# Optimization experiments

Measured on AMD Instinct MI355X. Metric: run time of the kernel, lower is better.

## Reference

```python
import jax, jax.numpy as jnp
import numpy as np

D, F, E, K = 1024, 2752, 8, 2  # hidden, intermediate, num_experts, top-k


def setup_inputs() -> dict:
    key = jax.random.key(0)
    k0, k1, k2, k3, k4 = jax.random.split(key, 5)
    s = 0.02  # init scale to keep activations in a sane range
    x = jax.random.normal(k0, (2, 512, D), jnp.float32)
    Ws = jax.random.normal(k1, (D, E), jnp.float32) * s
    bs = jnp.zeros((E,), jnp.float32)
    Wg = jax.random.normal(k2, (E, D, F), jnp.float32) * s
    Wu = jax.random.normal(k3, (E, D, F), jnp.float32) * s
    Wd = jax.random.normal(k4, (E, F, D), jnp.float32) * s
    return {"x": x, "Ws": Ws, "bs": bs, "Wg": Wg, "Wu": Wu, "Wd": Wd}


def reference(x, Ws, bs, Wg, Wu, Wd):
    b, n, d = x.shape
    xt = x.reshape(-1, d)                      # [T, D], T = b*n
    # gating: top-k over expert logits, softmax over the selected k
    logits = xt @ Ws + bs                      # [T, E]
    topk_w, topk_idx = jax.lax.top_k(logits, K)
    topk_w = jax.nn.softmax(topk_w, axis=-1)   # [T, K]
    # combine weights: zero for unselected experts
    combine = jnp.sum(jax.nn.one_hot(topk_idx, E, dtype=xt.dtype) * topk_w[..., None], axis=1)  # [T, E]
    # per-expert SwiGLU MLP (Llama): down(silu(gate(x)) * up(x))
    g = jnp.einsum('td,edf->tef', xt, Wg)
    u = jnp.einsum('td,edf->tef', xt, Wu)
    h = jax.nn.silu(g) * u                     # [T, E, F]
    y = jnp.einsum('tef,efd->ted', h, Wd)      # [T, E, D]
    out = jnp.einsum('ted,te->td', y, combine) # weighted combine over selected experts
    return out.reshape(b, n, d)
```

## Files before the change

kernel.cpp:

```cpp
#include <hip/hip_runtime.h>

#define DH 1024
#define FH 2752
#define NE 8
#define NT 1024
#define BM 256
#define BKF 64
#define BNF 32

typedef unsigned short u16;
typedef __bf16 bf16x8 __attribute__((ext_vector_type(8)));
typedef u16 u16x8 __attribute__((ext_vector_type(8)));
typedef float f32x4 __attribute__((ext_vector_type(4)));

__device__ __forceinline__ u16 f2bf(float f) {
  unsigned int u = __float_as_uint(f);
  unsigned int r = (u + 0x7fffu + ((u >> 16) & 1u)) >> 16;
  return (u16)r;
}
__device__ __forceinline__ float bf2f(u16 b) {
  return __uint_as_float(((unsigned int)b) << 16);
}
__device__ __forceinline__ bf16x8 as_bf(int4 v) {
  union { int4 i; bf16x8 b; } u; u.i = v; return u.b;
}
__device__ __forceinline__ bf16x8 as_bfu(u16x8 v) {
  union { u16x8 u; bf16x8 b; } x; x.u = v; return x.b;
}

__global__ void gate_kernel(const float* __restrict__ x,
                            const float* __restrict__ Ws,
                            const float* __restrict__ bs,
                            u16* __restrict__ xb,
                            int* __restrict__ tki,
                            float* __restrict__ tkw) {
  int gtid = blockIdx.x * blockDim.x + threadIdx.x;
  int t = gtid >> 6;
  int lane = gtid & 63;
  if (t >= NT) return;
  const float* xr = x + (size_t)t * DH;
  float acc[NE];
#pragma unroll
  for (int e = 0; e < NE; ++e) acc[e] = 0.f;
  for (int d = lane; d < DH; d += 64) {
    float xv = xr[d];
    xb[(size_t)t * DH + d] = f2bf(xv);
    const float4* wr = (const float4*)(Ws + (size_t)d * NE);
    float4 w0 = wr[0], w1 = wr[1];
    acc[0] += xv * w0.x; acc[1] += xv * w0.y;
    acc[2] += xv * w0.z; acc[3] += xv * w0.w;
    acc[4] += xv * w1.x; acc[5] += xv * w1.y;
    acc[6] += xv * w1.z; acc[7] += xv * w1.w;
  }
#pragma unroll
  for (int e = 0; e < NE; ++e) {
#pragma unroll
    for (int off = 32; off > 0; off >>= 1)
      acc[e] += __shfl_xor(acc[e], off);
  }
  if (lane == 0) {
    float l[NE];
#pragma unroll
    for (int e = 0; e < NE; ++e) l[e] = acc[e] + bs[e];
    int i0 = 0;
#pragma unroll
    for (int e = 1; e < NE; ++e) if (l[e] > l[i0]) i0 = e;
    int i1 = (i0 == 0) ? 1 : 0;
#pragma unroll
    for (int e = 0; e < NE; ++e) if (e != i0 && l[e] > l[i1]) i1 = e;
    float e1 = __expf(l[i1] - l[i0]);
    float denom = 1.f + e1;
    tki[t*2]   = i0; tki[t*2+1] = i1;
    tkw[t*2]   = 1.f / denom;
    tkw[t*2+1] = e1 / denom;
  }
}

__global__ void group_kernel(const int* __restrict__ tki,
                             int* __restrict__ offs,
                             int* __restrict__ rtok,
                             int* __restrict__ posf) {
  __shared__ int cnt[NE];
  __shared__ int run[NE];
  int tid = threadIdx.x;
  if (tid < NE) cnt[tid] = 0;
  __syncthreads();
  for (int t = tid; t < NT; t += blockDim.x) {
    atomicAdd(&cnt[tki[t*2]], 1);
    atomicAdd(&cnt[tki[t*2+1]], 1);
  }
  __syncthreads();
  if (tid == 0) {
    int r = 0;
    for (int e = 0; e < NE; ++e) { offs[e] = r; run[e] = r; r += cnt[e]; }
    offs[NE] = r;
  }
  __syncthreads();
  for (int t = tid; t < NT; t += blockDim.x) {
    for (int k = 0; k < 2; ++k) {
      int e = tki[t*2+k];
      int p = atomicAdd(&run[e], 1);
      rtok[p] = t;
      posf[t*2+k] = p;
    }
  }
}

#define GU_BODY(ACUR, ANXT, CUR, IT)                                          \
  {                                                                           \
    if ((IT) + 1 < 16) {                                                      \
      _Pragma("unroll") for (int h = 0; h < 2; ++h)                           \
      _Pragma("unroll") for (int i = 0; i < 4; ++i) {                         \
        bg_sm[(CUR)^1][ncB + i][klA + h] = f2bf(sg[h][i]);                    \
        bu_sm[(CUR)^1][ncB + i][klA + h] = f2bf(su[h][i]);                    \
      }                                                                       \
    }                                                                         \
    if ((IT) + 2 < 16) {                                                      \
      const float* g2 = gsrc + (size_t)((IT)+2) * BKF * FH;                   \
      const float* u2 = usrc + (size_t)((IT)+2) * BKF * FH;                   \
      sg[0] = *(const f32x4*)(g2);  sg[1] = *(const f32x4*)(g2 + FH);         \
      su[0] = *(const f32x4*)(u2);  su[1] = *(const f32x4*)(u2 + FH);         \
    }                                                                         \
    if ((IT) + 1 < 16) {                                                      \
      _Pragma("unroll") for (int mf = 0; mf < 4; ++mf) {                      \
        const u16* ap = aptr[mf] + ((IT)+1) * BKF;                            \
        ANXT[mf][0] = *(const int4*)(ap);                                     \
        ANXT[mf][1] = *(const int4*)(ap + 32);                                \
      }                                                                       \
    }                                                                         \
    _Pragma("unroll") for (int h = 0; h < 2; ++h) {                           \
      u16x8 fg0 = *(const u16x8*)&bg_sm[CUR][(lane&15)][h*32 + kg];           \
      u16x8 fg1 = *(const u16x8*)&bg_sm[CUR][16 + (lane&15)][h*32 + kg];      \
      u16x8 fu0 = *(const u16x8*)&bu_sm[CUR][(lane&15)][h*32 + kg];           \
      u16x8 fu1 = *(const u16x8*)&bu_sm[CUR][16 + (lane&15)][h*32 + kg];      \
      _Pragma("unroll") for (int mf = 0; mf < 4; ++mf) {                      \
        bf16x8 av = as_bf(ACUR[mf][h]);                                       \
        accg[mf][0] = __builtin_amdgcn_mfma_f32_16x16x32_bf16(av, as_bfu(fg0), accg[mf][0], 0,0,0); \
        accg[mf][1] = __builtin_amdgcn_mfma_f32_16x16x32_bf16(av, as_bfu(fg1), accg[mf][1], 0,0,0); \
        accu[mf][0] = __builtin_amdgcn_mfma_f32_16x16x32_bf16(av, as_bfu(fu0), accu[mf][0], 0,0,0); \
        accu[mf][1] = __builtin_amdgcn_mfma_f32_16x16x32_bf16(av, as_bfu(fu1), accu[mf][1], 0,0,0); \
      }                                                                       \
    }                                                                         \
    __syncthreads();                                                          \
  }

__global__ __launch_bounds__(256, 2)
void gu_kernel(const u16* __restrict__ xb,
               const float* __restrict__ Wg,
               const float* __restrict__ Wu,
               u16* __restrict__ hbuf,
               const int* __restrict__ offs,
               const int* __restrict__ rtok) {
  __shared__ u16 bg_sm[2][BNF][BKF + 8];
  __shared__ u16 bu_sm[2][BNF][BKF + 8];

  int e  = blockIdx.z;
  int mt = blockIdx.y;
  int nt = blockIdx.x;
  int off0 = offs[e];
  int cnt  = offs[e+1] - off0;
  if (cnt <= 0 || mt * BM >= cnt) return;
  int p0 = off0 + mt * BM;
  int rmax = cnt - mt * BM - 1;
  int n0 = nt * BNF;
  int tid = threadIdx.x;
  int lane = tid & 63, wv = tid >> 6;
  int kg = (lane >> 4) * 8;

  const u16* aptr[4];
#pragma unroll
  for (int mf = 0; mf < 4; ++mf) {
    int lrow = wv*64 + (lane & 15) + mf*16;
    int tok = rtok[p0 + (lrow > rmax ? rmax : lrow)];
    aptr[mf] = xb + (size_t)tok * DH + kg;
  }

  int klA = (tid >> 3) * 2;
  int ncB = (tid & 7) * 4;
  const float* gsrc = Wg + (size_t)e * DH * FH + (size_t)klA * FH + n0 + ncB;
  const float* usrc = Wu + (size_t)e * DH * FH + (size_t)klA * FH + n0 + ncB;

  f32x4 accg[4][2], accu[4][2];
#pragma unroll
  for (int mf = 0; mf < 4; ++mf)
#pragma unroll
    for (int nf = 0; nf < 2; ++nf) {
      accg[mf][nf] = f32x4{0.f,0.f,0.f,0.f};
      accu[mf][nf] = f32x4{0.f,0.f,0.f,0.f};
    }

  int4 a0[4][2], a1[4][2];
  f32x4 sg[2], su[2];

  sg[0] = *(const f32x4*)(gsrc);  sg[1] = *(const f32x4*)(gsrc + FH);
  su[0] = *(const f32x4*)(usrc);  su[1] = *(const f32x4*)(usrc + FH);
#pragma unroll
  for (int mf = 0; mf < 4; ++mf) {
    a0[mf][0] = *(const int4*)(aptr[mf]);
    a0[mf][1] = *(const int4*)(aptr[mf] + 32);
  }
#pragma unroll
  for (int h = 0; h < 2; ++h)
#pragma unroll
    for (int i = 0; i < 4; ++i) {
      bg_sm[0][ncB + i][klA + h] = f2bf(sg[h][i]);
      bu_sm[0][ncB + i][klA + h] = f2bf(su[h][i]);
    }
  {
    const float* g1 = gsrc + (size_t)BKF * FH;
    const float* u1 = usrc + (size_t)BKF * FH;
    sg[0] = *(const f32x4*)(g1);  sg[1] = *(const f32x4*)(g1 + FH);
    su[0] = *(const f32x4*)(u1);  su[1] = *(const f32x4*)(u1 + FH);
  }
  __syncthreads();

  for (int it = 0; it < 16; it += 2) {
    GU_BODY(a0, a1, 0, it);
    GU_BODY(a1, a0, 1, (it+1));
  }

#pragma unroll
  for (int mf = 0; mf < 4; ++mf) {
    int lr0 = wv*64 + (lane >> 4)*4 + mf*16;
#pragma unroll
    for (int nf = 0; nf < 2; ++nf) {
      int col = n0 + nf*16 + (lane & 15);
#pragma unroll
      for (int q = 0; q < 4; ++q) {
        int lrow = lr0 + q;
        if (lrow <= rmax) {
          float g = accg[mf][nf][q], u = accu[mf][nf][q];
          float s = g / (1.f + __expf(-g));
          hbuf[(size_t)(p0 + lrow) * FH + col] = f2bf(s * u);
        }
      }
    }
  }
}

#define DN_BODY(ACUR, ANXT, CUR, IT)                                          \
  {                                                                           \
    if ((IT) + 1 < nIter) {                                                   \
      _Pragma("unroll") for (int h = 0; h < 2; ++h)                           \
      _Pragma("unroll") for (int i = 0; i < 4; ++i)                           \
        b_sm[(CUR)^1][ncB + i][klA + h] = f2bf(sd[h][i]);                     \
    }                                                                         \
    if ((IT) + 2 < nIter) {                                                   \
      const float* d2 = dsrc + (size_t)((IT)+2) * BKF * DH;                   \
      sd[0] = *(const f32x4*)(d2);  sd[1] = *(const f32x4*)(d2 + DH);         \
    }                                                                         \
    if ((IT) + 1 < nIter) {                                                   \
      _Pragma("unroll") for (int mf = 0; mf < 4; ++mf) {                      \
        const u16* ap = aptr[mf] + ((IT)+1) * BKF;                            \
        ANXT[mf][0] = *(const int4*)(ap);                                     \
        ANXT[mf][1] = *(const int4*)(ap + 32);                                \
      }                                                                       \
    }                                                                         \
    _Pragma("unroll") for (int h = 0; h < 2; ++h) {                           \
      u16x8 f0 = *(const u16x8*)&b_sm[CUR][(lane&15)][h*32 + kg];             \
      u16x8 f1 = *(const u16x8*)&b_sm[CUR][16 + (lane&15)][h*32 + kg];        \
      _Pragma("unroll") for (int mf = 0; mf < 4; ++mf) {                      \
        bf16x8 av = as_bf(ACUR[mf][h]);                                       \
        acc[mf][0] = __builtin_amdgcn_mfma_f32_16x16x32_bf16(av, as_bfu(f0), acc[mf][0], 0,0,0); \
        acc[mf][1] = __builtin_amdgcn_mfma_f32_16x16x32_bf16(av, as_bfu(f1), acc[mf][1], 0,0,0); \
      }                                                                       \
    }                                                                         \
    __syncthreads();                                                          \
  }

__global__ __launch_bounds__(256, 2)
void dn_kernel(const u16* __restrict__ hb,
               const float* __restrict__ Wd,
               float* __restrict__ y,
               const int* __restrict__ offs) {
  __shared__ u16 b_sm[2][BNF][BKF + 8];

  int e  = blockIdx.z;
  int mt = blockIdx.y;
  int bx = blockIdx.x;
  int nt = bx & 31;
  int ks = bx >> 5;
  int kt0   = ks ? 1408 : 0;
  int nIter = ks ? 21 : 22;
  int off0 = offs[e];
  int cnt  = offs[e+1] - off0;
  if (cnt <= 0 || mt * BM >= cnt) return;
  int p0 = off0 + mt * BM;
  int rmax = cnt - mt * BM - 1;
  int n0 = nt * BNF;
  int tid = threadIdx.x;
  int lane = tid & 63, wv = tid >> 6;
  int kg = (lane >> 4) * 8;

  const u16* aptr[4];
#pragma unroll
  for (int mf = 0; mf < 4; ++mf) {
    int lrow = wv*64 + (lane & 15) + mf*16;
    int arow = p0 + (lrow > rmax ? rmax : lrow);
    aptr[mf] = hb + (size_t)arow * FH + kt0 + kg;
  }

  int klA = (tid >> 3) * 2;
  int ncB = (tid & 7) * 4;
  const float* dsrc = Wd + (size_t)e * FH * DH + (size_t)(kt0 + klA) * DH + n0 + ncB;

  f32x4 acc[4][2];
#pragma unroll
  for (int mf = 0; mf < 4; ++mf)
#pragma unroll
    for (int nf = 0; nf < 2; ++nf)
      acc[mf][nf] = f32x4{0.f,0.f,0.f,0.f};

  int4 a0[4][2], a1[4][2];
  f32x4 sd[2];

  sd[0] = *(const f32x4*)(dsrc);  sd[1] = *(const f32x4*)(dsrc + DH);
#pragma unroll
  for (int mf = 0; mf < 4; ++mf) {
    a0[mf][0] = *(const int4*)(aptr[mf]);
    a0[mf][1] = *(const int4*)(aptr[mf] + 32);
  }
#pragma unroll
  for (int h = 0; h < 2; ++h)
#pragma unroll
    for (int i = 0; i < 4; ++i)
      b_sm[0][ncB + i][klA + h] = f2bf(sd[h][i]);
  {
    const float* d1 = dsrc + (size_t)BKF * DH;
    sd[0] = *(const f32x4*)(d1);  sd[1] = *(const f32x4*)(d1 + DH);
  }
  __syncthreads();

  int it = 0;
  for (; it + 2 <= nIter; it += 2) {
    DN_BODY(a0, a1, 0, it);
    DN_BODY(a1, a0, 1, (it+1));
  }
  if (it < nIter) {
    DN_BODY(a0, a1, 0, it);
  }

  float* yout = y + (size_t)ks * 2048 * DH;
#pragma unroll
  for (int mf = 0; mf < 4; ++mf) {
    int lr0 = wv*64 + (lane >> 4)*4 + mf*16;
#pragma unroll
    for (int nf = 0; nf < 2; ++nf) {
      int col = n0 + nf*16 + (lane & 15);
#pragma unroll
      for (int q = 0; q < 4; ++q) {
        int lrow = lr0 + q;
        if (lrow <= rmax)
          yout[(size_t)(p0 + lrow) * DH + col] = acc[mf][nf][q];
      }
    }
  }
}

__global__ void combine_kernel(const float* __restrict__ y,
                               const float* __restrict__ tkw,
                               const int* __restrict__ posf,
                               float* __restrict__ out) {
  int t = blockIdx.x;
  int d = threadIdx.x;
  const float* y1 = y + (size_t)2048 * DH;
  int pa = posf[t*2], pb = posf[t*2+1];
  float wa = tkw[t*2], wb = tkw[t*2+1];
  f32x4 a0 = ((const f32x4*)(y  + (size_t)pa * DH))[d];
  f32x4 a1 = ((const f32x4*)(y1 + (size_t)pa * DH))[d];
  f32x4 b0 = ((const f32x4*)(y  + (size_t)pb * DH))[d];
  f32x4 b1 = ((const f32x4*)(y1 + (size_t)pb * DH))[d];
  f32x4 o;
#pragma unroll
  for (int i = 0; i < 4; ++i)
    o[i] = wa*(a0[i]+a1[i]) + wb*(b0[i]+b1[i]);
  ((f32x4*)(out + (size_t)t * DH))[d] = o;
}

extern "C" void kernel_launch(void* const* d_in, const int* in_sizes, int n_in,
                              void* d_out, int out_size, void* d_ws, size_t ws_size,
                              hipStream_t stream) {
  const float* x  = (const float*)d_in[0];
  const float* Ws = (const float*)d_in[1];
  const float* bs = (const float*)d_in[2];
  const float* Wg = (const float*)d_in[3];
  const float* Wu = (const float*)d_in[4];
  const float* Wd = (const float*)d_in[5];
  float* out = (float*)d_out;
  char* ws = (char*)d_ws;

  int*   tki  = (int*)  (ws + 0);
  float* tkw  = (float*)(ws + 8192);
  int*   offs = (int*)  (ws + 16384);
  int*   posf = (int*)  (ws + 20480);
  int*   rtok = (int*)  (ws + 28672);
  u16*   xb   = (u16*)  (ws + 36864);
  char*  base2 = ws + 36864 + 2097152;
  u16*   hbuf = (u16*)(base2);
  float* yws  = (float*)(base2 + 11272192);

  gate_kernel<<<256, 256, 0, stream>>>(x, Ws, bs, xb, tki, tkw);
  group_kernel<<<1, 256, 0, stream>>>(tki, offs, rtok, posf);
  gu_kernel<<<dim3(FH/BNF, 4, NE), 256, 0, stream>>>(xb, Wg, Wu, hbuf, offs, rtok);
  dn_kernel<<<dim3(64, 4, NE), 256, 0, stream>>>(hbuf, Wd, yws, offs);
  combine_kernel<<<NT, 256, 0, stream>>>(yws, tkw, posf, out);
}
```

Baseline: 185.5 us.

## Load weight fragments directly into registers, dropping LDS staging in expert GEMMs

Result: slower. 273.3 us (+47.3%).

```diff
diff --git a/kernel.cpp b/kernel.cpp
--- a/kernel.cpp
+++ b/kernel.cpp
@@ -5,8 +5,6 @@
 #define NE 8
 #define NT 1024
 #define BM 256
-#define BKF 64
-#define BNF 32
 
 typedef unsigned short u16;
 typedef __bf16 bf16x8 __attribute__((ext_vector_type(8)));
@@ -23,9 +21,6 @@
 }
 __device__ __forceinline__ bf16x8 as_bf(int4 v) {
   union { int4 i; bf16x8 b; } u; u.i = v; return u.b;
-}
-__device__ __forceinline__ bf16x8 as_bfu(u16x8 v) {
-  union { u16x8 u; bf16x8 b; } x; x.u = v; return x.b;
 }
 
 __global__ void gate_kernel(const float* __restrict__ x,
@@ -106,42 +101,32 @@
   }
 }
 
-#define GU_BODY(ACUR, ANXT, CUR, IT)                                          \
-  {                                                                           \
-    if ((IT) + 1 < 16) {                                                      \
-      _Pragma("unroll") for (int h = 0; h < 2; ++h)                           \
-      _Pragma("unroll") for (int i = 0; i < 4; ++i) {                         \
-        bg_sm[(CUR)^1][ncB + i][klA + h] = f2bf(sg[h][i]);                    \
-        bu_sm[(CUR)^1][ncB + i][klA + h] = f2bf(su[h][i]);                    \
-      }                                                                       \
-    }                                                                         \
-    if ((IT) + 2 < 16) {                                                      \
-      const float* g2 = gsrc + (size_t)((IT)+2) * BKF * FH;                   \
-      const float* u2 = usrc + (size_t)((IT)+2) * BKF * FH;                   \
-      sg[0] = *(const f32x4*)(g2);  sg[1] = *(const f32x4*)(g2 + FH);         \
-      su[0] = *(const f32x4*)(u2);  su[1] = *(const f32x4*)(u2 + FH);         \
-    }                                                                         \
-    if ((IT) + 1 < 16) {                                                      \
-      _Pragma("unroll") for (int mf = 0; mf < 4; ++mf) {                      \
-        const u16* ap = aptr[mf] + ((IT)+1) * BKF;                            \
-        ANXT[mf][0] = *(const int4*)(ap);                                     \
-        ANXT[mf][1] = *(const int4*)(ap + 32);                                \
-      }                                                                       \
-    }                                                                         \
-    _Pragma("unroll") for (int h = 0; h < 2; ++h) {                           \
-      u16x8 fg0 = *(const u16x8*)&bg_sm[CUR][(lane&15)][h*32 + kg];           \
-      u16x8 fg1 = *(const u16x8*)&bg_sm[CUR][16 + (lane&15)][h*32 + kg];      \
-      u16x8 fu0 = *(const u16x8*)&bu_sm[CUR][(lane&15)][h*32 + kg];           \
-      u16x8 fu1 = *(const u16x8*)&bu_sm[CUR][16 + (lane&15)][h*32 + kg];      \
-      _Pragma("unroll") for (int mf = 0; mf < 4; ++mf) {                      \
-        bf16x8 av = as_bf(ACUR[mf][h]);                                       \
-        accg[mf][0] = __builtin_amdgcn_mfma_f32_16x16x32_bf16(av, as_bfu(fg0), accg[mf][0], 0,0,0); \
-        accg[mf][1] = __builtin_amdgcn_mfma_f32_16x16x32_bf16(av, as_bfu(fg1), accg[mf][1], 0,0,0); \
-        accu[mf][0] = __builtin_amdgcn_mfma_f32_16x16x32_bf16(av, as_bfu(fu0), accu[mf][0], 0,0,0); \
-        accu[mf][1] = __builtin_amdgcn_mfma_f32_16x16x32_bf16(av, as_bfu(fu1), accu[mf][1], 0,0,0); \
-      }                                                                       \
-    }                                                                         \
-    __syncthreads();                                                          \
+#define GU_LOAD(ST, KT)                                                        \
+  {                                                                            \
+    int kb = (KT) * 32;                                                        \
+    _Pragma("unroll") for (int mf = 0; mf < 4; ++mf)                           \
+      A##ST[mf] = *(const int4*)(aptr[mf] + kb);                               \
+    _Pragma("unroll") for (int nf = 0; nf < 2; ++nf)                           \
+      _Pragma("unroll") for (int j = 0; j < 8; ++j) {                          \
+        Bg##ST[nf][j] = gcol[(kb + j) * FH + nf * 16];                         \
+        Bu##ST[nf][j] = ucol[(kb + j) * FH + nf * 16];                         \
+      }                                                                        \
+  }
+
+#define GU_COMPUTE(ST)                                                         \
+  {                                                                            \
+    _Pragma("unroll") for (int nf = 0; nf < 2; ++nf) {                         \
+      bf16x8 fg, fu;                                                           \
+      _Pragma("unroll") for (int j = 0; j < 8; ++j) {                          \
+        fg[j] = (__bf16)Bg##ST[nf][j];                                         \
+        fu[j] = (__bf16)Bu##ST[nf][j];                                         \
+      }                                                                        \
+      _Pragma("unroll") for (int mf = 0; mf < 4; ++mf) {                       \
+        bf16x8 av = as_bf(A##ST[mf]);                                          \
+        accg[mf][nf] = __builtin_amdgcn_mfma_f32_16x16x32_bf16(av, fg, accg[mf][nf], 0,0,0); \
+        accu[mf][nf] = __builtin_amdgcn_mfma_f32_16x16x32_bf16(av, fu, accu[mf][nf], 0,0,0); \
+      }                                                                        \
+    }                                                                          \
   }
 
 __global__ __launch_bounds__(256, 2)
@@ -151,9 +136,6 @@
                u16* __restrict__ hbuf,
                const int* __restrict__ offs,
                const int* __restrict__ rtok) {
-  __shared__ u16 bg_sm[2][BNF][BKF + 8];
-  __shared__ u16 bu_sm[2][BNF][BKF + 8];
-
   int e  = blockIdx.z;
   int mt = blockIdx.y;
   int nt = blockIdx.x;
@@ -162,23 +144,21 @@
   if (cnt <= 0 || mt * BM >= cnt) return;
   int p0 = off0 + mt * BM;
   int rmax = cnt - mt * BM - 1;
-  int n0 = nt * BNF;
+  int n0 = nt * 32;
   int tid = threadIdx.x;
   int lane = tid & 63, wv = tid >> 6;
   int kg = (lane >> 4) * 8;
+  int nl = lane & 15;
 
   const u16* aptr[4];
 #pragma unroll
   for (int mf = 0; mf < 4; ++mf) {
-    int lrow = wv*64 + (lane & 15) + mf*16;
+    int lrow = wv*64 + nl + mf*16;
     int tok = rtok[p0 + (lrow > rmax ? rmax : lrow)];
     aptr[mf] = xb + (size_t)tok * DH + kg;
   }
-
-  int klA = (tid >> 3) * 2;
-  int ncB = (tid & 7) * 4;
-  const float* gsrc = Wg + (size_t)e * DH * FH + (size_t)klA * FH + n0 + ncB;
-  const float* usrc = Wu + (size_t)e * DH * FH + (size_t)klA * FH + n0 + ncB;
+  const float* gcol = Wg + (size_t)e * DH * FH + (size_t)kg * FH + n0 + nl;
+  const float* ucol = Wu + (size_t)e * DH * FH + (size_t)kg * FH + n0 + nl;
 
   f32x4 accg[4][2], accu[4][2];
 #pragma unroll
@@ -189,34 +169,15 @@
       accu[mf][nf] = f32x4{0.f,0.f,0.f,0.f};
     }
 
-  int4 a0[4][2], a1[4][2];
-  f32x4 sg[2], su[2];
-
-  sg[0] = *(const f32x4*)(gsrc);  sg[1] = *(const f32x4*)(gsrc + FH);
-  su[0] = *(const f32x4*)(usrc);  su[1] = *(const f32x4*)(usrc + FH);
-#pragma unroll
-  for (int mf = 0; mf < 4; ++mf) {
-    a0[mf][0] = *(const int4*)(aptr[mf]);
-    a0[mf][1] = *(const int4*)(aptr[mf] + 32);
-  }
-#pragma unroll
-  for (int h = 0; h < 2; ++h)
-#pragma unroll
-    for (int i = 0; i < 4; ++i) {
-      bg_sm[0][ncB + i][klA + h] = f2bf(sg[h][i]);
-      bu_sm[0][ncB + i][klA + h] = f2bf(su[h][i]);
-    }
-  {
-    const float* g1 = gsrc + (size_t)BKF * FH;
-    const float* u1 = usrc + (size_t)BKF * FH;
-    sg[0] = *(const f32x4*)(g1);  sg[1] = *(const f32x4*)(g1 + FH);
-    su[0] = *(const f32x4*)(u1);  su[1] = *(const f32x4*)(u1 + FH);
-  }
-  __syncthreads();
-
-  for (int it = 0; it < 16; it += 2) {
-    GU_BODY(a0, a1, 0, it);
-    GU_BODY(a1, a0, 1, (it+1));
+  int4 A0[4], A1[4];
+  float Bg0[2][8], Bg1[2][8], Bu0[2][8], Bu1[2][8];
+
+  GU_LOAD(0, 0);
+  for (int t = 0; t < 32; t += 2) {
+    GU_LOAD(1, t+1);
+    GU_COMPUTE(0);
+    if (t + 2 < 32) GU_LOAD(0, t+2);
+    GU_COMPUTE(1);
   }
 
 #pragma unroll
@@ -224,7 +185,7 @@
     int lr0 = wv*64 + (lane >> 4)*4 + mf*16;
 #pragma unroll
     for (int nf = 0; nf < 2; ++nf) {
-      int col = n0 + nf*16 + (lane & 15);
+      int col = n0 + nf*16 + nl;
 #pragma unroll
       for (int q = 0; q < 4; ++q) {
         int lrow = lr0 + q;
@@ -238,34 +199,27 @@
   }
 }
 
-#define DN_BODY(ACUR, ANXT, CUR, IT)                                          \
-  {                                                                           \
-    if ((IT) + 1 < nIter) {                                                   \
-      _Pragma("unroll") for (int h = 0; h < 2; ++h)                           \
-      _Pragma("unroll") for (int i = 0; i < 4; ++i)                           \
-        b_sm[(CUR)^1][ncB + i][klA + h] = f2bf(sd[h][i]);                     \
-    }                                                                         \
-    if ((IT) + 2 < nIter) {                                                   \
-      const float* d2 = dsrc + (size_t)((IT)+2) * BKF * DH;                   \
-      sd[0] = *(const f32x4*)(d2);  sd[1] = *(const f32x4*)(d2 + DH);         \
-    }                                                                         \
-    if ((IT) + 1 < nIter) {                                                   \
-      _Pragma("unroll") for (int mf = 0; mf < 4; ++mf) {                      \
-        const u16* ap = aptr[mf] + ((IT)+1) * BKF;                            \
-        ANXT[mf][0] = *(const int4*)(ap);                                     \
-        ANXT[mf][1] = *(const int4*)(ap + 32);                                \
-      }                                                                       \
-    }                                                                         \
-    _Pragma("unroll") for (int h = 0; h < 2; ++h) {                           \
-      u16x8 f0 = *(const u16x8*)&b_sm[CUR][(lane&15)][h*32 + kg];             \
-      u16x8 f1 = *(const u16x8*)&b_sm[CUR][16 + (lane&15)][h*32 + kg];        \
-      _Pragma("unroll") for (int mf = 0; mf < 4; ++mf) {                      \
-        bf16x8 av = as_bf(ACUR[mf][h]);                                       \
-        acc[mf][0] = __builtin_amdgcn_mfma_f32_16x16x32_bf16(av, as_bfu(f0), acc[mf][0], 0,0,0); \
-        acc[mf][1] = __builtin_amdgcn_mfma_f32_16x16x32_bf16(av, as_bfu(f1), acc[mf][1], 0,0,0); \
-      }                                                                       \
-    }                                                                         \
-    __syncthreads();                                                          \
+#define DN_LOAD(ST, KT)                                                        \
+  {                                                                            \
+    int kb = (KT) * 32;                                                        \
+    _Pragma("unroll") for (int mf = 0; mf < 4; ++mf)                           \
+      A##ST[mf] = *(const int4*)(aptr[mf] + kb);                               \
+    _Pragma("unroll") for (int nf = 0; nf < 2; ++nf)                           \
+      _Pragma("unroll") for (int j = 0; j < 8; ++j)                            \
+        Bd##ST[nf][j] = dcol[(kb + j) * DH + nf * 16];                         \
+  }
+
+#define DN_COMPUTE(ST)                                                         \
+  {                                                                            \
+    _Pragma("unroll") for (int nf = 0; nf < 2; ++nf) {                         \
+      bf16x8 fd;                                                               \
+      _Pragma("unroll") for (int j = 0; j < 8; ++j)                            \
+        fd[j] = (__bf16)Bd##ST[nf][j];                                         \
+      _Pragma("unroll") for (int mf = 0; mf < 4; ++mf) {                       \
+        bf16x8 av = as_bf(A##ST[mf]);                                          \
+        acc[mf][nf] = __builtin_amdgcn_mfma_f32_16x16x32_bf16(av, fd, acc[mf][nf], 0,0,0); \
+      }                                                                        \
+    }                                                                          \
   }
 
 __global__ __launch_bounds__(256, 2)
@@ -273,36 +227,31 @@
                const float* __restrict__ Wd,
                float* __restrict__ y,
                const int* __restrict__ offs) {
-  __shared__ u16 b_sm[2][BNF][BKF + 8];
-
   int e  = blockIdx.z;
   int mt = blockIdx.y;
   int bx = blockIdx.x;
   int nt = bx & 31;
   int ks = bx >> 5;
-  int kt0   = ks ? 1408 : 0;
-  int nIter = ks ? 21 : 22;
+  int kt0 = ks * 1376;
   int off0 = offs[e];
   int cnt  = offs[e+1] - off0;
   if (cnt <= 0 || mt * BM >= cnt) return;
   int p0 = off0 + mt * BM;
   int rmax = cnt - mt * BM - 1;
-  int n0 = nt * BNF;
+  int n0 = nt * 32;
   int tid = threadIdx.x;
   int lane = tid & 63, wv = tid >> 6;
   int kg = (lane >> 4) * 8;
+  int nl = lane & 15;
 
   const u16* aptr[4];
 #pragma unroll
   for (int mf = 0; mf < 4; ++mf) {
-    int lrow = wv*64 + (lane & 15) + mf*16;
+    int lrow = wv*64 + nl + mf*16;
     int arow = p0 + (lrow > rmax ? rmax : lrow);
     aptr[mf] = hb + (size_t)arow * FH + kt0 + kg;
   }
-
-  int klA = (tid >> 3) * 2;
-  int ncB = (tid & 7) * 4;
-  const float* dsrc = Wd + (size_t)e * FH * DH + (size_t)(kt0 + klA) * DH + n0 + ncB;
+  const float* dcol = Wd + (size_t)e * FH * DH + (size_t)(kt0 + kg) * DH + n0 + nl;
 
   f32x4 acc[4][2];
 #pragma unroll
@@ -311,34 +260,18 @@
     for (int nf = 0; nf < 2; ++nf)
       acc[mf][nf] = f32x4{0.f,0.f,0.f,0.f};
 
-  int4 a0[4][2], a1[4][2];
-  f32x4 sd[2];
-
-  sd[0] = *(const f32x4*)(dsrc);  sd[1] = *(const f32x4*)(dsrc + DH);
-#pragma unroll
-  for (int mf = 0; mf < 4; ++mf) {
-    a0[mf][0] = *(const int4*)(aptr[mf]);
-    a0[mf][1] = *(const int4*)(aptr[mf] + 32);
-  }
-#pragma unroll
-  for (int h = 0; h < 2; ++h)
-#pragma unroll
-    for (int i = 0; i < 4; ++i)
-      b_sm[0][ncB + i][klA + h] = f2bf(sd[h][i]);
-  {
-    const float* d1 = dsrc + (size_t)BKF * DH;
-    sd[0] = *(const f32x4*)(d1);  sd[1] = *(const f32x4*)(d1 + DH);
-  }
-  __syncthreads();
-
-  int it = 0;
-  for (; it + 2 <= nIter; it += 2) {
-    DN_BODY(a0, a1, 0, it);
-    DN_BODY(a1, a0, 1, (it+1));
-  }
-  if (it < nIter) {
-    DN_BODY(a0, a1, 0, it);
-  }
+  int4 A0[4], A1[4];
+  float Bd0[2][8], Bd1[2][8];
+
+  DN_LOAD(0, 0);
+  int t = 0;
+  for (; t + 2 <= 43; t += 2) {
+    DN_LOAD(1, t+1);
+    DN_COMPUTE(0);
+    if (t + 2 < 43) DN_LOAD(0, t+2);
+    DN_COMPUTE(1);
+  }
+  DN_COMPUTE(0);
 
   float* yout = y + (size_t)ks * 2048 * DH;
 #pragma unroll
@@ -346,7 +279,7 @@
     int lr0 = wv*64 + (lane >> 4)*4 + mf*16;
 #pragma unroll
     for (int nf = 0; nf < 2; ++nf) {
-      int col = n0 + nf*16 + (lane & 15);
+      int col = n0 + nf*16 + nl;
 #pragma unroll
       for (int q = 0; q < 4; ++q) {
         int lrow = lr0 + q;
@@ -401,7 +334,7 @@
 
   gate_kernel<<<256, 256, 0, stream>>>(x, Ws, bs, xb, tki, tkw);
   group_kernel<<<1, 256, 0, stream>>>(tki, offs, rtok, posf);
-  gu_kernel<<<dim3(FH/BNF, 4, NE), 256, 0, stream>>>(xb, Wg, Wu, hbuf, offs, rtok);
+  gu_kernel<<<dim3(FH/32, 4, NE), 256, 0, stream>>>(xb, Wg, Wu, hbuf, offs, rtok);
   dn_kernel<<<dim3(64, 4, NE), 256, 0, stream>>>(hbuf, Wd, yws, offs);
   combine_kernel<<<NT, 256, 0, stream>>>(yws, tkw, posf, out);
 }
```
